# Kernel tuning notes

Measured on AMD Instinct MI355X. Metric: run time of the kernel, lower is better.

## Reference

```python
import jax, jax.numpy as jnp
import numpy as np

TOP_K = 2


def setup_inputs() -> dict:
    key = jax.random.key(0)
    k0, k1, k2, k3, k4 = jax.random.split(key, 5)
    B, S, D, F, E = 4, 2048, 2048, 1408, 8
    scale = 0.02
    return {
        "hidden_states": jax.random.normal(k0, (B, S, D), jnp.float32),
        "router_w": jax.random.normal(k1, (D, E), jnp.float32) * scale,
        "w_gate": jax.random.normal(k2, (E, D, F), jnp.float32) * scale,
        "w_up": jax.random.normal(k3, (E, D, F), jnp.float32) * scale,
        "w_down": jax.random.normal(k4, (E, F, D), jnp.float32) * scale,
    }


def reference(hidden_states, router_w, w_gate, w_up, w_down):
    B, S, D = hidden_states.shape
    x = hidden_states.reshape(-1, D)              # [N, D]
    N = x.shape[0]
    E = router_w.shape[-1]

    # ---- Router: softmax over experts, top-k, renormalize top-k probs ----
    logits = x @ router_w                         # [N, E]
    probs = jax.nn.softmax(logits, axis=-1)
    top_w, top_i = jax.lax.top_k(probs, TOP_K)    # [N, K]
    top_w = top_w / jnp.sum(top_w, axis=-1, keepdims=True)

    # Dense gate matrix [N, E]: gate is the (renormalized) routing weight for
    # selected experts, zero otherwise.
    gates = jnp.zeros_like(probs).at[jnp.arange(N)[:, None], top_i].set(top_w)

    # ---- Load-balancing aux loss (Switch-style, averaged over top-k) ----
    f = jnp.mean(jnp.sum(jax.nn.one_hot(top_i, E, dtype=x.dtype), axis=1), axis=0)  # [E] dispatch fraction
    P = jnp.mean(probs, axis=0)                   # [E] mean router prob
    aux_loss = (E / TOP_K) * jnp.sum(f * P)

    # ---- Per-expert SwiGLU FFN, computed as grouped GEMMs over all experts ----
    g = jnp.einsum("nd,edf->enf", x, w_gate)      # [E, N, F]
    u = jnp.einsum("nd,edf->enf", x, w_up)        # [E, N, F]
    h = jax.nn.silu(g) * u                        # [E, N, F]
    expert_out = jnp.einsum("enf,efd->end", h, w_down)  # [E, N, D]

    # ---- Combine: gate-weighted sum over experts ----
    out = jnp.einsum("ne,end->nd", gates, expert_out)   # [N, D]
    return out.reshape(B, S, D), aux_loss
```

## Files before the change

kernel.cpp:

```cpp
#include <hip/hip_runtime.h>

#define N_TOK 8192
#define DIM   2048
#define FFN   1408

#define XGP_OFF 0ull
#define P1_OFF  71303168ull
#define P2_OFF  163577856ull
#define HP_OFF  209715200ull
#define LPK_OFF 258736128ull
#define LW_OFF  258801664ull
#define TI_OFF  258867200ull
#define TW_OFF  258899968ull
#define ST_OFF  258932736ull

typedef __bf16 bf16x8 __attribute__((ext_vector_type(8)));
typedef float  f32x4  __attribute__((ext_vector_type(4)));
typedef int    int4v  __attribute__((ext_vector_type(4)));
typedef __attribute__((address_space(1))) void as1_void;
typedef __attribute__((address_space(3))) void as3_void;

__device__ __forceinline__ void gload16(const void* g, void* l) {
  __builtin_amdgcn_global_load_lds((as1_void*)g, (as3_void*)l, 16, 0, 0);
}

__device__ __forceinline__ ushort f2bf(float f) {
  unsigned u = __builtin_bit_cast(unsigned, f);
  u += 0x7FFFu + ((u >> 16) & 1u);
  return (ushort)(u >> 16);
}

__device__ __forceinline__ int4v dsread(int addr) {
  int4v d;
  asm volatile("ds_read_b128 %0, %1" : "=v"(d) : "v"(addr));
  return d;
}

#define WAITL() do { asm volatile("s_waitcnt lgkmcnt(0)" ::: "memory"); \
                     __builtin_amdgcn_sched_barrier(0); } while (0)
#define BAR()   __builtin_amdgcn_s_barrier()
#define MFMA16(a, b, c) __builtin_amdgcn_mfma_f32_16x16x32_bf16(a, b, c, 0, 0, 0)
#define BC(x) __builtin_bit_cast(bf16x8, x)

__device__ __forceinline__ int swz(int row, int s) {
  int q = row >> 1;
  int p = (((row & 1) << 2) | s) ^ (q & 7);
  return q * 128 + p * 16;
}

__global__ __launch_bounds__(256) void router_kernel(
    const float* __restrict__ x, const float* __restrict__ rw,
    int* __restrict__ topi, float* __restrict__ topw,
    int* __restrict__ cnt, unsigned long long* __restrict__ psum)
{
  int tid = threadIdx.x, lane = tid & 63, wv = tid >> 6;
  __shared__ float sP[4][8];
  __shared__ int   sC[4][8];
  float pacc[8]; int cacc[8];
  #pragma unroll
  for (int e = 0; e < 8; ++e) { pacc[e] = 0.f; cacc[e] = 0; }

  #pragma unroll 1
  for (int it = 0; it < 4; ++it) {
    int t = blockIdx.x * 16 + wv * 4 + it;
    const float4* xr = (const float4*)(x + (size_t)t * DIM);
    float acc[8];
    #pragma unroll
    for (int e = 0; e < 8; ++e) acc[e] = 0.f;
    #pragma unroll 1
    for (int i = 0; i < 8; ++i) {
      int j = i * 64 + lane;
      float4 v = xr[j];
      const float* rr = rw + (size_t)j * 32;
      #pragma unroll
      for (int c = 0; c < 4; ++c) {
        float xv = (&v.x)[c];
        const float4* r4 = (const float4*)(rr + c * 8);
        float4 q0 = r4[0], q1 = r4[1];
        acc[0] += xv * q0.x; acc[1] += xv * q0.y; acc[2] += xv * q0.z; acc[3] += xv * q0.w;
        acc[4] += xv * q1.x; acc[5] += xv * q1.y; acc[6] += xv * q1.z; acc[7] += xv * q1.w;
      }
    }
    #pragma unroll
    for (int off = 32; off; off >>= 1) {
      #pragma unroll
      for (int e = 0; e < 8; ++e) acc[e] += __shfl_xor(acc[e], off);
    }
    float m = acc[0];
    #pragma unroll
    for (int e = 1; e < 8; ++e) m = fmaxf(m, acc[e]);
    float p[8], s = 0.f;
    #pragma unroll
    for (int e = 0; e < 8; ++e) { p[e] = __expf(acc[e] - m); s += p[e]; }
    float inv = 1.f / s;
    int i1 = 0; float p1 = p[0];
    #pragma unroll
    for (int e = 1; e < 8; ++e) if (p[e] > p1) { p1 = p[e]; i1 = e; }
    int i2 = -1; float p2 = -1.f;
    #pragma unroll
    for (int e = 0; e < 8; ++e) if (e != i1 && p[e] > p2) { p2 = p[e]; i2 = e; }
    float w1 = p1 / (p1 + p2);
    if (lane == 0) {
      topi[t] = i1 | (i2 << 8);
      topw[t] = w1;
      #pragma unroll
      for (int e = 0; e < 8; ++e) pacc[e] += p[e] * inv;
      cacc[i1]++; cacc[i2]++;
    }
  }
  if (lane == 0) {
    #pragma unroll
    for (int e = 0; e < 8; ++e) { sP[wv][e] = pacc[e]; sC[wv][e] = cacc[e]; }
  }
  __syncthreads();
  if (tid < 8) {
    float ps = sP[0][tid] + sP[1][tid] + sP[2][tid] + sP[3][tid];
    int   cs = sC[0][tid] + sC[1][tid] + sC[2][tid] + sC[3][tid];
    atomicAdd(&cnt[tid], cs);
    atomicAdd(&psum[tid], (unsigned long long)((double)ps * 1099511627776.0));
  }
}

__global__ void scan_aux_kernel(int* __restrict__ stats,
                                const unsigned long long* __restrict__ psum,
                                float* __restrict__ aux_out)
{
  if (threadIdx.x == 0 && blockIdx.x == 0) {
    int b = 0, tb = 0;
    for (int e = 0; e < 8; ++e) {
      stats[8 + e] = b; stats[16 + e] = b; stats[24 + e] = tb;
      tb += (stats[e] + 127) >> 7;
      b += stats[e];
    }
    stats[32] = tb;
    double s = 0.0;
    for (int e = 0; e < 8; ++e)
      s += (double)stats[e] * ((double)psum[e] * (1.0 / 1099511627776.0));
    aux_out[0] = (float)(4.0 * s / ((double)N_TOK * (double)N_TOK));
  }
}

__global__ __launch_bounds__(256) void place_kernel(
    const int* __restrict__ topi, const float* __restrict__ topw,
    int* __restrict__ stats, int* __restrict__ lpk, float* __restrict__ lw)
{
  int t = blockIdx.x * 256 + threadIdx.x;
  if (t >= N_TOK) return;
  int pk = topi[t];
  int e1 = pk & 0xff, e2 = (pk >> 8) & 0xff;
  float w1 = topw[t];
  int p1 = atomicAdd(&stats[8 + e1], 1);
  lpk[p1] = (t << 1); lw[p1] = w1;
  int p2 = atomicAdd(&stats[8 + e2], 1);
  lpk[p2] = (t << 1) | 1; lw[p2] = 1.f - w1;
}

__global__ __launch_bounds__(256) void gather_x_kernel(
    const float* __restrict__ x, const int* __restrict__ lpk,
    const int* __restrict__ stats, char* __restrict__ xgp)
{
  int b = blockIdx.x;
  if (b >= stats[32]) return;
  int e = 0;
  #pragma unroll
  for (int k = 1; k < 8; ++k) if (b >= stats[24 + k]) e = k;
  int tloc = b - stats[24 + e];
  int abase = stats[16 + e], Me = stats[e];
  int lane = threadIdx.x & 63, wv = threadIdx.x >> 6;
  char* base = xgp + (size_t)b * 64 * 8192;
  #pragma unroll 1
  for (int r = wv; r < 128; r += 4) {
    int lrow = tloc * 128 + r;
    bool valid = lrow < Me;
    const float* src = x + (valid ? (size_t)(lpk[abase + lrow] >> 1) * DIM : 0);
    int q = r >> 1;
    #pragma unroll
    for (int it = 0; it < 4; ++it) {
      int c16 = it * 64 + lane;
      int j = c16 >> 2, s = c16 & 3;
      ushort u8[8];
      if (valid) {
        float4 v0 = *(const float4*)(src + c16 * 8);
        float4 v1 = *(const float4*)(src + c16 * 8 + 4);
        u8[0] = f2bf(v0.x); u8[1] = f2bf(v0.y); u8[2] = f2bf(v0.z); u8[3] = f2bf(v0.w);
        u8[4] = f2bf(v1.x); u8[5] = f2bf(v1.y); u8[6] = f2bf(v1.z); u8[7] = f2bf(v1.w);
      } else {
        #pragma unroll
        for (int i = 0; i < 8; ++i) u8[i] = 0;
      }
      int p = (((r & 1) << 2) | s) ^ (q & 7);
      char* d = base + (size_t)j * 8192 + q * 128 + p * 16;
      *(ushort4*)d = *(ushort4*)&u8[0];
      *(ushort4*)(d + 8) = *(ushort4*)&u8[4];
    }
  }
}

__global__ __launch_bounds__(256) void pack_gu_kernel(
    const float* __restrict__ wg, const float* __restrict__ wu, char* __restrict__ p1)
{
  int j = blockIdx.x, tn = blockIdx.y, e = blockIdx.z;
  __shared__ float tg[32][65];
  __shared__ float tu[32][65];
  int t = threadIdx.x;
  const float* gs = wg + ((size_t)e * DIM + j * 32) * FFN + tn * 64;
  const float* us = wu + ((size_t)e * DIM + j * 32) * FFN + tn * 64;
  #pragma unroll
  for (int k2 = 0; k2 < 2; ++k2) {
    int idx = t + k2 * 256;
    int kk = idx >> 4, fq = idx & 15;
    *(float4*)&tg[kk][fq * 4] = *(const float4*)(gs + (size_t)kk * FFN + fq * 4);
    *(float4*)&tu[kk][fq * 4] = *(const float4*)(us + (size_t)kk * FFN + fq * 4);
  }
  __syncthreads();
  char* dst = p1 + ((size_t)((e * 22 + tn) * 64 + j)) * 8192;
  #pragma unroll
  for (int k2 = 0; k2 < 2; ++k2) {
    int L = t + k2 * 256;
    int q = L >> 3, v = (L & 7) ^ (q & 7);
    int r = 2 * q + (v >> 2), s = v & 3;
    const float* col = (r < 64) ? &tg[s * 8][r] : &tu[s * 8][r - 64];
    ushort u8[8];
    #pragma unroll
    for (int i = 0; i < 8; ++i) u8[i] = f2bf(col[i * 65]);
    *(ushort4*)(dst + (size_t)L * 16) = *(ushort4*)&u8[0];
    *(ushort4*)(dst + (size_t)L * 16 + 8) = *(ushort4*)&u8[4];
  }
}

__global__ __launch_bounds__(256) void pack_d_kernel(
    const float* __restrict__ wd, char* __restrict__ p2)
{
  int j = blockIdx.x, tn = blockIdx.y, e = blockIdx.z;
  __shared__ float t2[32][129];
  int t = threadIdx.x;
  const float* src = wd + ((size_t)e * FFN + j * 32) * DIM + tn * 128;
  #pragma unroll
  for (int k2 = 0; k2 < 4; ++k2) {
    int idx = t + k2 * 256;
    int kk = idx >> 5, dq = idx & 31;
    *(float4*)&t2[kk][dq * 4] = *(const float4*)(src + (size_t)kk * DIM + dq * 4);
  }
  __syncthreads();
  char* dst = p2 + ((size_t)((e * 16 + tn) * 44 + j)) * 8192;
  #pragma unroll
  for (int k2 = 0; k2 < 2; ++k2) {
    int L = t + k2 * 256;
    int q = L >> 3, v = (L & 7) ^ (q & 7);
    int r = 2 * q + (v >> 2), s = v & 3;
    ushort u8[8];
    #pragma unroll
    for (int i = 0; i < 8; ++i) u8[i] = f2bf(t2[s * 8 + i][r]);
    *(ushort4*)(dst + (size_t)L * 16) = *(ushort4*)&u8[0];
    *(ushort4*)(dst + (size_t)L * 16 + 8) = *(ushort4*)&u8[4];
  }
}


#define GSTAGE(AC, BC_, BUF) do { int d_ = (BUF) * 16384 + wv * 2048; \
  gload16((AC) + wv * 2048 + lane * 16, sm + d_); \
  gload16((AC) + wv * 2048 + 1024 + lane * 16, sm + d_ + 1024); \
  gload16((BC_) + wv * 2048 + lane * 16, sm + d_ + 8192); \
  gload16((BC_) + wv * 2048 + 1024 + lane * 16, sm + d_ + 8192 + 1024); \
} while (0)

#define KLOOP(NCH) \
  GSTAGE(aP, bP, 0); \
  _Pragma("unroll 1") \
  for (int j = 0; j < (NCH); ++j) { \
    if (j + 1 < (NCH)) { \
      GSTAGE(aP + (size_t)(j + 1) * 8192, bP + (size_t)(j + 1) * 8192, (j + 1) & 1); \
      asm volatile("s_waitcnt vmcnt(4)" ::: "memory"); \
    } else { \
      asm volatile("s_waitcnt vmcnt(0)" ::: "memory"); \
    } \
    BAR(); \
    int sb = (j & 1) * 16384; \
    int4v va[4], vb[4]; \
    _Pragma("unroll") for (int n = 0; n < 4; ++n) vb[n] = dsread(sb + adB[n]); \
    _Pragma("unroll") for (int m = 0; m < 4; ++m) va[m] = dsread(sb + adA[m]); \
    WAITL(); \
    __builtin_amdgcn_s_setprio(1); \
    _Pragma("unroll") for (int m = 0; m < 4; ++m) \
      _Pragma("unroll") for (int n = 0; n < 4; ++n) \
        acc[m][n] = MFMA16(BC(va[m]), BC(vb[n]), acc[m][n]); \
    __builtin_amdgcn_s_setprio(0); \
    BAR(); \
  }

__global__ __launch_bounds__(256, 4) void gemm_gu_kernel(
    const char* __restrict__ xgp, const char* __restrict__ p1,
    const int* __restrict__ stats, char* __restrict__ hp)
{
  int bid = blockIdx.x;
  int e = bid & 7;
  int Ll = bid >> 3;
  int tm = Ll / 22, tn = Ll % 22;
  int Me = stats[e];
  if (tm * 128 >= Me) return;
  int tb = stats[24 + e];

  __shared__ char sm[32768];
  int tid = threadIdx.x, lane = tid & 63, wv = tid >> 6;
  const char* aP = xgp + (size_t)(tb + tm) * 64 * 8192;
  const char* bP = p1 + (size_t)((e * 22 + tn) * 64) * 8192;

  int wm = wv >> 1, wn = wv & 1, s = lane >> 4;
  int adA[4], adB[4];
  #pragma unroll
  for (int m = 0; m < 4; ++m) adA[m] = swz(wm * 64 + m * 16 + (lane & 15), s);
  #pragma unroll
  for (int n = 0; n < 4; ++n) adB[n] = 8192 + swz(wn * 64 + n * 16 + (lane & 15), s);

  f32x4 acc[4][4];
  #pragma unroll
  for (int m = 0; m < 4; ++m)
    #pragma unroll
    for (int n = 0; n < 4; ++n) acc[m][n] = (f32x4){0, 0, 0, 0};

  KLOOP(64);

  float* u_lds = (float*)sm;
  if (wn == 1) {
    #pragma unroll
    for (int m = 0; m < 4; ++m)
      #pragma unroll
      for (int n = 0; n < 4; ++n)
        #pragma unroll
        for (int r = 0; r < 4; ++r) {
          int row = wm * 64 + m * 16 + (lane >> 4) * 4 + r;
          int c = n * 16 + (lane & 15);
          u_lds[row * 64 + c] = acc[m][n][r];
        }
  }
  __syncthreads();
  if (wn == 0) {
    char* hb = hp + (size_t)(tb + tm) * 44 * 8192;
    #pragma unroll
    for (int m = 0; m < 4; ++m)
      #pragma unroll
      for (int n = 0; n < 4; ++n)
        #pragma unroll
        for (int r = 0; r < 4; ++r) {
          int row = wm * 64 + m * 16 + (lane >> 4) * 4 + r;
          int c = n * 16 + (lane & 15);
          float g = acc[m][n][r];
          float u = u_lds[row * 64 + c];
          float hv = g * u / (1.f + __expf(-g));
          int f = tn * 64 + c;
          int j2 = f >> 5, s2 = (f >> 3) & 3, i2 = f & 7;
          int q = row >> 1;
          int p = (((row & 1) << 2) | s2) ^ (q & 7);
          *(ushort*)(hb + (size_t)j2 * 8192 + q * 128 + p * 16 + i2 * 2) = f2bf(hv);
        }
  }
}

__global__ __launch_bounds__(256, 4) void gemm_down_kernel(
    const char* __restrict__ hp, const char* __restrict__ p2,
    const int* __restrict__ lpk, const float* __restrict__ lw,
    const int* __restrict__ stats, float* __restrict__ out)
{
  int bid = blockIdx.x;
  int e = bid & 7;
  int Ll = bid >> 3;
  int tm = Ll >> 4, tn = Ll & 15;
  int Me = stats[e];
  if (tm * 128 >= Me) return;
  int tb = stats[24 + e], abase = stats[16 + e];

  __shared__ char sm[32768];
  int tid = threadIdx.x, lane = tid & 63, wv = tid >> 6;
  const char* aP = hp + (size_t)(tb + tm) * 44 * 8192;
  const char* bP = p2 + (size_t)((e * 16 + tn) * 44) * 8192;

  int wm = wv >> 1, wn = wv & 1, s = lane >> 4;
  int adA[4], adB[4];
  #pragma unroll
  for (int m = 0; m < 4; ++m) adA[m] = swz(wm * 64 + m * 16 + (lane & 15), s);
  #pragma unroll
  for (int n = 0; n < 4; ++n) adB[n] = 8192 + swz(wn * 64 + n * 16 + (lane & 15), s);

  f32x4 acc[4][4];
  #pragma unroll
  for (int m = 0; m < 4; ++m)
    #pragma unroll
    for (int n = 0; n < 4; ++n) acc[m][n] = (f32x4){0, 0, 0, 0};

  KLOOP(44);

  int c0 = lane & 15, r0 = (lane >> 4) * 4;
  #pragma unroll
  for (int m = 0; m < 4; ++m) {
    #pragma unroll
    for (int r = 0; r < 4; ++r) {
      int lrow = tm * 128 + wm * 64 + m * 16 + r0 + r;
      if (lrow < Me) {
        int t = lpk[abase + lrow] >> 1;
        float w = lw[abase + lrow];
        #pragma unroll
        for (int n = 0; n < 4; ++n) {
          int col = tn * 128 + wn * 64 + n * 16 + c0;
          unsafeAtomicAdd(&out[(size_t)t * DIM + col], w * acc[m][n][r]);
        }
      }
    }
  }
}

extern "C" void kernel_launch(void* const* d_in, const int* in_sizes, int n_in,
                              void* d_out, int out_size, void* d_ws, size_t ws_size,
                              hipStream_t stream)
{
  const float* x  = (const float*)d_in[0];
  const float* rw = (const float*)d_in[1];
  const float* wg = (const float*)d_in[2];
  const float* wu = (const float*)d_in[3];
  const float* wd = (const float*)d_in[4];
  float* out = (float*)d_out;

  char* ws = (char*)d_ws;
  char*   xgp  = ws + XGP_OFF;
  char*   p1   = ws + P1_OFF;
  char*   p2   = ws + P2_OFF;
  char*   hp   = ws + HP_OFF;
  int*    lpk  = (int*)(ws + LPK_OFF);
  float*  lw   = (float*)(ws + LW_OFF);
  int*    topi = (int*)(ws + TI_OFF);
  float*  topw = (float*)(ws + TW_OFF);
  int*    stats = (int*)(ws + ST_OFF);
  unsigned long long* psum = (unsigned long long*)(ws + ST_OFF + 192);

  hipMemsetAsync(d_out, 0, (size_t)out_size * sizeof(float), stream);
  hipMemsetAsync(ws + ST_OFF, 0, 256, stream);

  router_kernel<<<512, 256, 0, stream>>>(x, rw, topi, topw, stats, psum);
  scan_aux_kernel<<<1, 64, 0, stream>>>(stats, psum, out + (size_t)out_size - 1);
  place_kernel<<<32, 256, 0, stream>>>(topi, topw, stats, lpk, lw);

  gather_x_kernel<<<136, 256, 0, stream>>>(x, lpk, stats, xgp);
  pack_gu_kernel<<<dim3(64, 22, 8), 256, 0, stream>>>(wg, wu, p1);
  pack_d_kernel<<<dim3(44, 16, 8), 256, 0, stream>>>(wd, p2);

  gemm_gu_kernel<<<5632, 256, 0, stream>>>(xgp, p1, stats, hp);
  gemm_down_kernel<<<4096, 256, 0, stream>>>(hp, p2, lpk, lw, stats, out);
}
```

Baseline: 624.6 us.

## Replace atomic scatter-add combine with per-slot expert output and combine kernel

The down-projection GEMM now writes plain per-slot expert outputs into a workspace buffer instead of doing atomic adds into the output. A new combine kernel reads each token's two slots via a token-to-position map and writes the weighted sum directly, which also removes the output memset. Separately, the router now emits a bf16 copy of x so the gather kernel copies bf16 rows instead of re-reading and converting fp32. This adds an extra 16K x 2048 fp32 round trip through memory and one more launch in exchange for removing atomic contention and halving the gather read traffic.

```diff
diff --git a/kernel.cpp b/kernel.cpp
--- a/kernel.cpp
+++ b/kernel.cpp
@@ -4,14 +4,16 @@
 #define DIM   2048
 #define FFN   1408
 
-#define XGP_OFF 0ull
-#define P1_OFF  71303168ull
-#define P2_OFF  163577856ull
-#define HP_OFF  209715200ull
+#define XB_OFF  0ull
+#define HP_OFF  0ull
+#define XGP_OFF 49020928ull
+#define P1_OFF  120324096ull
+#define EO_OFF  49020928ull
+#define P2_OFF  212598784ull
 #define LPK_OFF 258736128ull
-#define LW_OFF  258801664ull
-#define TI_OFF  258867200ull
-#define TW_OFF  258899968ull
+#define TI_OFF  258801664ull
+#define TW_OFF  258834432ull
+#define TP_OFF  258867200ull
 #define ST_OFF  258932736ull
 
 typedef __bf16 bf16x8 __attribute__((ext_vector_type(8)));
@@ -50,7 +52,7 @@
 
 __global__ __launch_bounds__(256) void router_kernel(
     const float* __restrict__ x, const float* __restrict__ rw,
-    int* __restrict__ topi, float* __restrict__ topw,
+    ushort* __restrict__ xb, int* __restrict__ topi, float* __restrict__ topw,
     int* __restrict__ cnt, unsigned long long* __restrict__ psum)
 {
   int tid = threadIdx.x, lane = tid & 63, wv = tid >> 6;
@@ -71,6 +73,8 @@
     for (int i = 0; i < 8; ++i) {
       int j = i * 64 + lane;
       float4 v = xr[j];
+      ushort4 o; o.x = f2bf(v.x); o.y = f2bf(v.y); o.z = f2bf(v.z); o.w = f2bf(v.w);
+      *(ushort4*)(xb + (size_t)t * DIM + (size_t)j * 4) = o;
       const float* rr = rw + (size_t)j * 32;
       #pragma unroll
       for (int c = 0; c < 4; ++c) {
@@ -141,22 +145,22 @@
 }
 
 __global__ __launch_bounds__(256) void place_kernel(
-    const int* __restrict__ topi, const float* __restrict__ topw,
-    int* __restrict__ stats, int* __restrict__ lpk, float* __restrict__ lw)
+    const int* __restrict__ topi, int* __restrict__ stats,
+    int* __restrict__ lpk, int2* __restrict__ tpos)
 {
   int t = blockIdx.x * 256 + threadIdx.x;
   if (t >= N_TOK) return;
   int pk = topi[t];
   int e1 = pk & 0xff, e2 = (pk >> 8) & 0xff;
-  float w1 = topw[t];
   int p1 = atomicAdd(&stats[8 + e1], 1);
-  lpk[p1] = (t << 1); lw[p1] = w1;
+  lpk[p1] = t;
   int p2 = atomicAdd(&stats[8 + e2], 1);
-  lpk[p2] = (t << 1) | 1; lw[p2] = 1.f - w1;
+  lpk[p2] = t;
+  tpos[t] = make_int2(p1, p2);
 }
 
 __global__ __launch_bounds__(256) void gather_x_kernel(
-    const float* __restrict__ x, const int* __restrict__ lpk,
+    const ushort* __restrict__ xb, const int* __restrict__ lpk,
     const int* __restrict__ stats, char* __restrict__ xgp)
 {
   int b = blockIdx.x;
@@ -172,26 +176,17 @@
   for (int r = wv; r < 128; r += 4) {
     int lrow = tloc * 128 + r;
     bool valid = lrow < Me;
-    const float* src = x + (valid ? (size_t)(lpk[abase + lrow] >> 1) * DIM : 0);
+    const char* src = (const char*)xb + (valid ? (size_t)lpk[abase + lrow] * (DIM * 2) : 0);
     int q = r >> 1;
     #pragma unroll
     for (int it = 0; it < 4; ++it) {
       int c16 = it * 64 + lane;
       int j = c16 >> 2, s = c16 & 3;
-      ushort u8[8];
-      if (valid) {
-        float4 v0 = *(const float4*)(src + c16 * 8);
-        float4 v1 = *(const float4*)(src + c16 * 8 + 4);
-        u8[0] = f2bf(v0.x); u8[1] = f2bf(v0.y); u8[2] = f2bf(v0.z); u8[3] = f2bf(v0.w);
-        u8[4] = f2bf(v1.x); u8[5] = f2bf(v1.y); u8[6] = f2bf(v1.z); u8[7] = f2bf(v1.w);
-      } else {
-        #pragma unroll
-        for (int i = 0; i < 8; ++i) u8[i] = 0;
-      }
+      uint4 v;
+      if (valid) v = *(const uint4*)(src + c16 * 16);
+      else       v = make_uint4(0, 0, 0, 0);
       int p = (((r & 1) << 2) | s) ^ (q & 7);
-      char* d = base + (size_t)j * 8192 + q * 128 + p * 16;
-      *(ushort4*)d = *(ushort4*)&u8[0];
-      *(ushort4*)(d + 8) = *(ushort4*)&u8[4];
+      *(uint4*)(base + (size_t)j * 8192 + q * 128 + p * 16) = v;
     }
   }
 }
@@ -358,8 +353,7 @@
 
 __global__ __launch_bounds__(256, 4) void gemm_down_kernel(
     const char* __restrict__ hp, const char* __restrict__ p2,
-    const int* __restrict__ lpk, const float* __restrict__ lw,
-    const int* __restrict__ stats, float* __restrict__ out)
+    const int* __restrict__ stats, float* __restrict__ eo)
 {
   int bid = blockIdx.x;
   int e = bid & 7;
@@ -396,15 +390,34 @@
     for (int r = 0; r < 4; ++r) {
       int lrow = tm * 128 + wm * 64 + m * 16 + r0 + r;
       if (lrow < Me) {
-        int t = lpk[abase + lrow] >> 1;
-        float w = lw[abase + lrow];
+        float* dst = eo + (size_t)(abase + lrow) * DIM + tn * 128 + wn * 64 + c0;
         #pragma unroll
-        for (int n = 0; n < 4; ++n) {
-          int col = tn * 128 + wn * 64 + n * 16 + c0;
-          unsafeAtomicAdd(&out[(size_t)t * DIM + col], w * acc[m][n][r]);
-        }
+        for (int n = 0; n < 4; ++n) dst[n * 16] = acc[m][n][r];
       }
     }
+  }
+}
+
+__global__ __launch_bounds__(256) void combine_kernel(
+    const float* __restrict__ eo, const int2* __restrict__ tpos,
+    const float* __restrict__ topw, float* __restrict__ out)
+{
+  int t = blockIdx.x;
+  int2 tp = tpos[t];
+  float w1 = topw[t], w2 = 1.f - w1;
+  const float4* r1 = (const float4*)(eo + (size_t)tp.x * DIM);
+  const float4* r2 = (const float4*)(eo + (size_t)tp.y * DIM);
+  float4* o = (float4*)(out + (size_t)t * DIM);
+  #pragma unroll
+  for (int k = 0; k < 2; ++k) {
+    int i = threadIdx.x + k * 256;
+    float4 a = r1[i], b = r2[i];
+    float4 c;
+    c.x = w1 * a.x + w2 * b.x;
+    c.y = w1 * a.y + w2 * b.y;
+    c.z = w1 * a.z + w2 * b.z;
+    c.w = w1 * a.w + w2 * b.w;
+    o[i] = c;
   }
 }
 
@@ -420,28 +433,31 @@
   float* out = (float*)d_out;
 
   char* ws = (char*)d_ws;
+  ushort* xb   = (ushort*)(ws + XB_OFF);
+  char*   hp   = ws + HP_OFF;
   char*   xgp  = ws + XGP_OFF;
   char*   p1   = ws + P1_OFF;
+  float*  eo   = (float*)(ws + EO_OFF);
   char*   p2   = ws + P2_OFF;
-  char*   hp   = ws + HP_OFF;
   int*    lpk  = (int*)(ws + LPK_OFF);
-  float*  lw   = (float*)(ws + LW_OFF);
   int*    topi = (int*)(ws + TI_OFF);
   float*  topw = (float*)(ws + TW_OFF);
+  int2*   tpos = (int2*)(ws + TP_OFF);
   int*    stats = (int*)(ws + ST_OFF);
   unsigned long long* psum = (unsigned long long*)(ws + ST_OFF + 192);
 
-  hipMemsetAsync(d_out, 0, (size_t)out_size * sizeof(float), stream);
   hipMemsetAsync(ws + ST_OFF, 0, 256, stream);
 
-  router_kernel<<<512, 256, 0, stream>>>(x, rw, topi, topw, stats, psum);
+  router_kernel<<<512, 256, 0, stream>>>(x, rw, xb, topi, topw, stats, psum);
   scan_aux_kernel<<<1, 64, 0, stream>>>(stats, psum, out + (size_t)out_size - 1);
-  place_kernel<<<32, 256, 0, stream>>>(topi, topw, stats, lpk, lw);
-
-  gather_x_kernel<<<136, 256, 0, stream>>>(x, lpk, stats, xgp);
+  place_kernel<<<32, 256, 0, stream>>>(topi, stats, lpk, tpos);
+
+  gather_x_kernel<<<136, 256, 0, stream>>>(xb, lpk, stats, xgp);
   pack_gu_kernel<<<dim3(64, 22, 8), 256, 0, stream>>>(wg, wu, p1);
   pack_d_kernel<<<dim3(44, 16, 8), 256, 0, stream>>>(wd, p2);
 
   gemm_gu_kernel<<<5632, 256, 0, stream>>>(xgp, p1, stats, hp);
-  gemm_down_kernel<<<4096, 256, 0, stream>>>(hp, p2, lpk, lw, stats, out);
-}
+  gemm_down_kernel<<<4096, 256, 0, stream>>>(hp, p2, stats, eo);
+
+  combine_kernel<<<8192, 256, 0, stream>>>(eo, tpos, topw, out);
+}
```

Measured after the change: 581.9 us. -6.8%, faster.
